# Kernel optimization log

Hardware: AMD Instinct MI355X
Metric: run time of the kernel (lower is better)

## Reference

```python
import jax, jax.numpy as jnp
import numpy as np

A, OBS, TD, H, M, ACT, AE = 1024, 2048, 256, 128, 16, 256, 64


def setup_inputs() -> dict:
    key = jax.random.key(0)
    ks = jax.random.split(key, 16)
    p = lambda k, shape: jax.random.normal(k, shape, dtype=jnp.float32) * 0.02
    obs = jax.random.normal(ks[0], (A, OBS), dtype=jnp.float32)
    # group membership matrix: exactly M members per initiator row (ATOC top-m groups)
    scores = jax.random.uniform(ks[1], (A, A))
    idx = jnp.argsort(scores, axis=1)[:, :M]
    C = jnp.zeros((A, A), dtype=bool).at[jnp.arange(A)[:, None], idx].set(True)
    inp = dict(obs=obs, C=C)
    # actor_1: Linear(OBS,TD) -> LN -> ReLU -> Linear(TD,TD) -> LN
    inp['W1'] = p(ks[2], (OBS, TD)); inp['b1'] = jnp.zeros((TD,), jnp.float32)
    inp['g1'] = jnp.ones((TD,), jnp.float32); inp['bt1'] = jnp.zeros((TD,), jnp.float32)
    inp['W2'] = p(ks[3], (TD, TD)); inp['b2'] = jnp.zeros((TD,), jnp.float32)
    inp['g2'] = jnp.ones((TD,), jnp.float32); inp['bt2'] = jnp.zeros((TD,), jnp.float32)
    # attention unit: 2-layer MLP + sigmoid head
    inp['aW1'] = p(ks[4], (TD, AE)); inp['ab1'] = jnp.zeros((AE,), jnp.float32)
    inp['aW2'] = p(ks[5], (AE, AE)); inp['ab2'] = jnp.zeros((AE,), jnp.float32)
    inp['aW3'] = p(ks[6], (AE, 1)); inp['ab3'] = jnp.zeros((1,), jnp.float32)
    # bi-directional LSTM (PyTorch layout: W_ih [4H,TD], W_hh [4H,H])
    inp['Wih_f'] = p(ks[7], (4 * H, TD)); inp['Whh_f'] = p(ks[8], (4 * H, H))
    inp['bih_f'] = jnp.zeros((4 * H,), jnp.float32); inp['bhh_f'] = jnp.zeros((4 * H,), jnp.float32)
    inp['Wih_r'] = p(ks[9], (4 * H, TD)); inp['Whh_r'] = p(ks[10], (4 * H, H))
    inp['bih_r'] = jnp.zeros((4 * H,), jnp.float32); inp['bhh_r'] = jnp.zeros((4 * H,), jnp.float32)
    # actor_2: ReLU -> Linear(TD,TD) -> LN -> Linear(TD,ACT) -> LN -> Tanh
    inp['W3'] = p(ks[11], (TD, TD)); inp['b3'] = jnp.zeros((TD,), jnp.float32)
    inp['g3'] = jnp.ones((TD,), jnp.float32); inp['bt3'] = jnp.zeros((TD,), jnp.float32)
    inp['W4'] = p(ks[12], (TD, ACT)); inp['b4'] = jnp.zeros((ACT,), jnp.float32)
    inp['g4'] = jnp.ones((ACT,), jnp.float32); inp['bt4'] = jnp.zeros((ACT,), jnp.float32)
    return inp


def _ln(x, g, b, eps=1e-5):
    m = jnp.mean(x, -1, keepdims=True)
    v = jnp.mean((x - m) ** 2, -1, keepdims=True)
    return (x - m) * jax.lax.rsqrt(v + eps) * g + b


def _lstm(seq, Wih, Whh, bih, bhh):
    # seq [T, D] -> hidden outputs [T, H]; PyTorch gate order i, f, g, o
    def step(carry, x):
        h, c = carry
        z = x @ Wih.T + bih + h @ Whh.T + bhh
        i, f, g, o = jnp.split(z, 4)
        c = jax.nn.sigmoid(f) * c + jax.nn.sigmoid(i) * jnp.tanh(g)
        h = jax.nn.sigmoid(o) * jnp.tanh(c)
        return (h, c), h
    h0 = jnp.zeros((H,), seq.dtype)
    _, hs = jax.lax.scan(step, (h0, h0), seq)
    return hs


def _forward(obs, C, W1, b1, g1, bt1, W2, b2, g2, bt2, aW1, ab1, aW2, ab2, aW3, ab3,
             Wih_f, Whh_f, bih_f, bhh_f, Wih_r, Whh_r, bih_r, bhh_r,
             W3, b3, g3, bt3, W4, b4, g4, bt4):
    # actor_1
    t = jax.nn.relu(_ln(obs @ W1 + b1, g1, bt1))
    thoughts = _ln(t @ W2 + b2, g2, bt2)  # [A, TD]
    # attention unit -> initiators (threshold 0.5)
    a = jax.nn.relu(thoughts @ aW1 + ab1)
    a = jax.nn.relu(a @ aW2 + ab2)
    init_prob = jax.nn.sigmoid(a @ aW3 + ab3)[:, 0]
    is_init = init_prob > 0.5  # [A]
    tpos = jnp.arange(M)

    def comm_step(th, xs):
        mask, active = xs
        # members first (stable, increasing agent index), padded gather of size M
        order = jnp.argsort((~mask).astype(jnp.int32))[:M]
        gcnt = jnp.sum(mask).astype(jnp.int32)
        seq_f = th[order]                        # [M, TD]
        rev = jnp.clip(gcnt - 1 - tpos, 0, M - 1)
        seq_b = seq_f[rev]                       # valid prefix reversed
        out_f = _lstm(seq_f, Wih_f, Whh_f, bih_f, bhh_f)
        out_b = _lstm(seq_b, Wih_r, Whh_r, bih_r, bhh_r)
        out = jnp.concatenate([out_f, out_b[rev]], axis=-1)  # [M, TD] bi-LSTM aligned
        valid = (tpos < gcnt) & active
        newv = jnp.where(valid[:, None], out, seq_f)         # merge = replace by integrated
        return th.at[order].set(newv), None

    thoughts, _ = jax.lax.scan(comm_step, thoughts, (C, is_init))
    # actor_2
    h = jax.nn.relu(thoughts)
    h = _ln(h @ W3 + b3, g3, bt3)
    acts = jnp.tanh(_ln(h @ W4 + b4, g4, bt4))
    return acts


def reference(obs, C, W1, b1, g1, bt1, W2, b2, g2, bt2, aW1, ab1, aW2, ab2, aW3, ab3,
              Wih_f, Whh_f, bih_f, bhh_f, Wih_r, Whh_r, bih_r, bhh_r,
              W3, b3, g3, bt3, W4, b4, g4, bt4):
    return _forward(obs, C, W1, b1, g1, bt1, W2, b2, g2, bt2, aW1, ab1, aW2, ab2, aW3, ab3,
                    Wih_f, Whh_f, bih_f, bhh_f, Wih_r, Whh_r, bih_r, bhh_r,
                    W3, b3, g3, bt3, W4, b4, g4, bt4)
```

## Files before the change

### kernel.cpp

```cpp
#include <hip/hip_runtime.h>
#include <cstdint>
#include <cstddef>
#include <math.h>

#define A_N   1024
#define OBS_N 2048
#define TD_N  256
#define H_N   128
#define M_N   16
#define AE_N  64
#define NWGC  32

typedef _Float16 h2 __attribute__((ext_vector_type(2)));
typedef _Float16 f16x8 __attribute__((ext_vector_type(8)));
typedef float f32x4 __attribute__((ext_vector_type(4)));

__device__ __forceinline__ float sigf(float x) { return 1.0f / (1.0f + expf(-x)); }
__device__ __forceinline__ h2 u2h(unsigned int u) { union { unsigned int x; h2 h; } c; c.x = u; return c.h; }
__device__ __forceinline__ unsigned int packh(float a, float b) {
  union { h2 h; unsigned int u; } c;
  c.h = (h2){(_Float16)a, (_Float16)b};
  return c.u;
}

__device__ __forceinline__ bool c_at(const unsigned char* C, int as_int, size_t idx) {
  return as_int ? (((const int*)C)[idx] != 0) : (C[idx] != 0);
}

__global__ __launch_bounds__(64) void k_cdet(const unsigned char* __restrict__ C, int* __restrict__ flag) {
  int lane = threadIdx.x;
  int cnt = 0;
  for (int i = lane; i < 4096; i += 64) cnt += (C[i] != 0) ? 1 : 0;
  for (int off = 32; off; off >>= 1) cnt += __shfl_down(cnt, off);
  if (lane == 0) flag[0] = (cnt < 40) ? 1 : 0;
}

__global__ __launch_bounds__(256) void k_actor1a(const float* __restrict__ obs,
    const float* __restrict__ W1, const float* __restrict__ b1,
    const float* __restrict__ g1, const float* __restrict__ bt1,
    float* __restrict__ tout) {
  __shared__ float S[4 * OBS_N];
  __shared__ float red[4][4][2];
  int tid = threadIdx.x;
  int r0 = blockIdx.x * 4;
  {
    const float4* src = (const float4*)(obs + (size_t)r0 * OBS_N);
    float4* dst = (float4*)S;
    for (int i = tid; i < 4 * OBS_N / 4; i += 256) dst[i] = src[i];
  }
  __syncthreads();
  int j = tid;
  float acc0 = 0, acc1 = 0, acc2 = 0, acc3 = 0;
  const float4* S4 = (const float4*)S;
  for (int k4 = 0; k4 < OBS_N / 4; k4++) {
    float w0 = W1[(k4 * 4 + 0) * TD_N + j];
    float w1 = W1[(k4 * 4 + 1) * TD_N + j];
    float w2 = W1[(k4 * 4 + 2) * TD_N + j];
    float w3 = W1[(k4 * 4 + 3) * TD_N + j];
    float4 s0 = S4[0 * 512 + k4], s1 = S4[1 * 512 + k4], s2 = S4[2 * 512 + k4], s3 = S4[3 * 512 + k4];
    acc0 += s0.x * w0 + s0.y * w1 + s0.z * w2 + s0.w * w3;
    acc1 += s1.x * w0 + s1.y * w1 + s1.z * w2 + s1.w * w3;
    acc2 += s2.x * w0 + s2.y * w1 + s2.z * w2 + s2.w * w3;
    acc3 += s3.x * w0 + s3.y * w1 + s3.z * w2 + s3.w * w3;
  }
  float z[4] = {acc0 + b1[j], acc1 + b1[j], acc2 + b1[j], acc3 + b1[j]};
  int w = tid >> 6, lane = tid & 63;
  for (int r = 0; r < 4; r++) {
    float v = z[r], v2 = z[r] * z[r];
    for (int off = 32; off; off >>= 1) { v += __shfl_down(v, off); v2 += __shfl_down(v2, off); }
    if (lane == 0) { red[r][w][0] = v; red[r][w][1] = v2; }
  }
  __syncthreads();
  for (int r = 0; r < 4; r++) {
    float sm = red[r][0][0] + red[r][1][0] + red[r][2][0] + red[r][3][0];
    float sq = red[r][0][1] + red[r][1][1] + red[r][2][1] + red[r][3][1];
    float mean = sm * (1.0f / TD_N);
    float var = sq * (1.0f / TD_N) - mean * mean;
    float rs = 1.0f / sqrtf(var + 1e-5f);
    float val = (z[r] - mean) * rs * g1[j] + bt1[j];
    tout[(size_t)(r0 + r) * TD_N + j] = fmaxf(val, 0.0f);
  }
}

__global__ __launch_bounds__(256) void k_actor1b(const float* __restrict__ tin,
    const float* __restrict__ W2, const float* __restrict__ b2,
    const float* __restrict__ g2, const float* __restrict__ bt2,
    float* __restrict__ th) {
  __shared__ float S[4 * TD_N];
  __shared__ float red[4][4][2];
  int tid = threadIdx.x;
  int r0 = blockIdx.x * 4;
  for (int i = tid; i < 4 * TD_N; i += 256) S[i] = tin[(size_t)r0 * TD_N + i];
  __syncthreads();
  int j = tid;
  float z[4] = {0, 0, 0, 0};
  const float4* S4 = (const float4*)S;
  for (int k4 = 0; k4 < TD_N / 4; k4++) {
    float w0 = W2[(k4 * 4 + 0) * TD_N + j];
    float w1 = W2[(k4 * 4 + 1) * TD_N + j];
    float w2v = W2[(k4 * 4 + 2) * TD_N + j];
    float w3 = W2[(k4 * 4 + 3) * TD_N + j];
#pragma unroll
    for (int r = 0; r < 4; r++) {
      float4 sv = S4[r * 64 + k4];
      z[r] += sv.x * w0 + sv.y * w1 + sv.z * w2v + sv.w * w3;
    }
  }
  for (int r = 0; r < 4; r++) z[r] += b2[j];
  int w = tid >> 6, lane = tid & 63;
  for (int r = 0; r < 4; r++) {
    float v = z[r], v2 = z[r] * z[r];
    for (int off = 32; off; off >>= 1) { v += __shfl_down(v, off); v2 += __shfl_down(v2, off); }
    if (lane == 0) { red[r][w][0] = v; red[r][w][1] = v2; }
  }
  __syncthreads();
  for (int r = 0; r < 4; r++) {
    float sm = red[r][0][0] + red[r][1][0] + red[r][2][0] + red[r][3][0];
    float sq = red[r][0][1] + red[r][1][1] + red[r][2][1] + red[r][3][1];
    float mean = sm * (1.0f / TD_N);
    float var = sq * (1.0f / TD_N) - mean * mean;
    float rs = 1.0f / sqrtf(var + 1e-5f);
    th[(size_t)(r0 + r) * TD_N + j] = (z[r] - mean) * rs * g2[j] + bt2[j];
  }
}

__global__ __launch_bounds__(256) void k_att(const float* __restrict__ th,
    const float* __restrict__ aW1, const float* __restrict__ ab1,
    const float* __restrict__ aW2, const float* __restrict__ ab2,
    const float* __restrict__ aW3, const float* __restrict__ ab3,
    int* __restrict__ isin) {
  __shared__ float S[4 * TD_N];
  __shared__ double A1[4 * AE_N];
  __shared__ double A2[4 * AE_N];
  int tid = threadIdx.x;
  int r0 = blockIdx.x * 4;
  for (int i = tid; i < 4 * TD_N; i += 256) S[i] = th[(size_t)r0 * TD_N + i];
  __syncthreads();
  int r = tid >> 6, c = tid & 63;
  double acc = 0;
  for (int k = 0; k < TD_N; k++) acc += (double)S[r * TD_N + k] * (double)aW1[k * AE_N + c];
  acc += (double)ab1[c];
  A1[r * AE_N + c] = acc > 0.0 ? acc : 0.0;
  __syncthreads();
  acc = 0;
  for (int k = 0; k < AE_N; k++) acc += A1[r * AE_N + k] * (double)aW2[k * AE_N + c];
  acc += (double)ab2[c];
  A2[r * AE_N + c] = acc > 0.0 ? acc : 0.0;
  __syncthreads();
  double p = A2[r * AE_N + c] * (double)aW3[c];
  for (int off = 32; off; off >>= 1) p += __shfl_down(p, off);
  if (c == 0) isin[r0 + r] = ((p + (double)ab3[0]) > 0.0) ? 1 : 0;
}

__global__ __launch_bounds__(64) void k_memb(const unsigned char* __restrict__ C,
    const int* __restrict__ flag, int* __restrict__ memb) {
  int s = blockIdx.x, lane = threadIdx.x;
  int as_int = flag[0];
  if (lane < M_N) memb[s * M_N + lane] = lane;
  __syncthreads();
  int base = 0;
  for (int ch = 0; ch < 16; ch++) {
    int col = ch * 64 + lane;
    bool v = c_at(C, as_int, (size_t)s * A_N + col);
    unsigned long long m = __ballot(v);
    if (v) {
      int pos = base + __popcll(m & ((1ull << lane) - 1ull));
      if (pos < M_N) memb[s * M_N + pos] = col;
    }
    base += __popcll(m);
  }
}

__global__ __launch_bounds__(256) void k_req(const unsigned char* __restrict__ C,
    const int* __restrict__ flag, const int* __restrict__ memb,
    const int* __restrict__ isin, int* __restrict__ req) {
  __shared__ int Ls[A_N];
  int s = blockIdx.x, tid = threadIdx.x;
  int as_int = flag[0];
  for (int i = tid; i < A_N; i += 256) Ls[i] = isin[i];
  __syncthreads();
  int i = tid >> 4, sub = tid & 15;
  int m = memb[s * M_N + i] & (A_N - 1);
  int cnt = 0;
  for (int s2 = sub; s2 < s; s2 += 16)
    if (Ls[s2] && c_at(C, as_int, (size_t)s2 * A_N + m)) cnt++;
  for (int off = 1; off < 16; off <<= 1) cnt += __shfl_xor(cnt, off);
  if (sub == 0) req[s * M_N + i] = cnt;
}

__global__ __launch_bounds__(256) void k_prep(
    const float* __restrict__ Wih_f, const float* __restrict__ Wih_r,
    const float* __restrict__ Whh_f, const float* __restrict__ Whh_r,
    const float* __restrict__ bih_f, const float* __restrict__ bhh_f,
    const float* __restrict__ bih_r, const float* __restrict__ bhh_r,
    unsigned int* __restrict__ wfragf, unsigned int* __restrict__ wfragr,
    unsigned int* __restrict__ whhpf, unsigned int* __restrict__ whhpr,
    float* __restrict__ bsumf, float* __restrict__ bsumr,
    int* __restrict__ verF, int* __restrict__ verB) {
  int id = blockIdx.x * 256 + threadIdx.x;
  if (id < 65536) {
    int j = id & 3, l = (id >> 2) & 63, tile = (id >> 8) & 31, c = id >> 13;
    int gate = tile * 16 + (l & 15);
    int k = c * 32 + ((l >> 4) << 3) + (j << 1);
    wfragf[id] = packh(Wih_f[gate * TD_N + k], Wih_f[gate * TD_N + k + 1]);
    wfragr[id] = packh(Wih_r[gate * TD_N + k], Wih_r[gate * TD_N + k + 1]);
  }
  if (id < 32768) {
    int g = id & 511, k2 = id >> 9;
    whhpf[id] = packh(Whh_f[g * H_N + 2 * k2], Whh_f[g * H_N + 2 * k2 + 1]);
    whhpr[id] = packh(Whh_r[g * H_N + 2 * k2], Whh_r[g * H_N + 2 * k2 + 1]);
  }
  if (id < 512) { bsumf[id] = bih_f[id] + bhh_f[id]; bsumr[id] = bih_r[id] + bhh_r[id]; }
  if (id < A_N) { verF[id] = 0; verB[id] = 0; }
}

__global__ __launch_bounds__(64) void k_lvl(const int* __restrict__ isin,
    const int* __restrict__ memb, int* __restrict__ fin,
    int* __restrict__ lstart, int* __restrict__ llist) {
  __shared__ int membS[A_N * M_N];
  __shared__ int last[A_N];
  __shared__ int cnt[A_N + 2];
  __shared__ int cur[A_N + 2];
  __shared__ short lvlS[A_N];
  __shared__ unsigned char isinS[A_N];
  __shared__ unsigned char cntm[A_N];
  int lane = threadIdx.x;
  for (int i = lane; i < A_N * M_N; i += 64) membS[i] = memb[i] & (A_N - 1);
  for (int i = lane; i < A_N; i += 64) {
    isinS[i] = (unsigned char)(isin[i] != 0);
    last[i] = 0; cntm[i] = 0; lvlS[i] = 0;
  }
  for (int l = lane; l < A_N + 2; l += 64) cnt[l] = 0;
  __syncthreads();
  for (int s = 0; s < A_N; s++) {
    if (isinS[s]) {
      int li = 0, m = 0;
      if (lane < 16) { m = membS[s * M_N + lane]; li = last[m]; }
#pragma unroll
      for (int off = 8; off; off >>= 1) li = max(li, __shfl_xor(li, off));
      int L = __shfl(li, 0) + 1;
      if (lane < 16) { last[m] = L; cntm[m]++; }
      if (lane == 0) { lvlS[s] = (short)L; cnt[L]++; }
    }
  }
  if (lane == 0) {
    int acc = 0;
    for (int L = 1; L <= A_N; L++) { cur[L] = acc; acc += cnt[L]; }
    lstart[0] = acc;
    for (int s = 0; s < A_N; s++) {
      int L = lvlS[s];
      if (L > 0) llist[cur[L]++] = s;
    }
  }
  for (int i = lane; i < A_N; i += 64) fin[i] = cntm[i] & 1;
}

#define RSH 264
__global__ __launch_bounds__(512)
void k_scan(
    float* __restrict__ thA, float* __restrict__ thB,
    const int* __restrict__ lstart, const int* __restrict__ llist,
    const int* __restrict__ memb, const int* __restrict__ req,
    int* __restrict__ verF, int* __restrict__ verB,
    const unsigned int* __restrict__ wfragf, const unsigned int* __restrict__ wfragr,
    const unsigned int* __restrict__ whhpf, const unsigned int* __restrict__ whhpr,
    const float* __restrict__ bsumf, const float* __restrict__ bsumr) {
  __shared__ __align__(16) unsigned short Sh[16 * RSH];
  __shared__ float xa_lds[16 * 512 + 7936];
  __shared__ float hh[16 * H_N];
  __shared__ float garr[4 * H_N];
  __shared__ unsigned int hp[2 * 64];
  __shared__ int memb_s[16];
  __shared__ int par_s[16];
  int tid = threadIdx.x;
  int wg = blockIdx.x;
  int dir = wg & 1;
  int pair = wg >> 1;
  int dmask = dir ? 15 : 0;
  const unsigned int* wfrag = dir ? wfragr : wfragf;
  const unsigned int* whhp = dir ? whhpr : whhpf;
  float blo = (dir ? bsumr : bsumf)[tid];
  int istanh = ((tid >> 7) == 2);
  int* vown = dir ? verB : verF;
  int wv = tid >> 6, lane = tid & 63;
  int fm = lane & 15, fkg = lane >> 4;
  unsigned int wreg[64];
#pragma unroll
  for (int k2 = 0; k2 < 64; k2++) wreg[k2] = whhp[k2 * 512 + tid];
#pragma unroll
  for (int k2 = 0; k2 < 64; k2++) asm volatile("" : "+v"(wreg[k2]));

  int nact = lstart[0];
  for (int idx = pair; idx < nact; idx += NWGC / 2) {
    int s = llist[idx];
    if (tid < 16) {
      int m = memb[s * M_N + tid] & (A_N - 1);
      int rq = req[s * M_N + tid];
      memb_s[tid] = m;
      par_s[tid] = rq & 1;
      int tries = 0;
      while (__hip_atomic_load(&verF[m], __ATOMIC_RELAXED, __HIP_MEMORY_SCOPE_AGENT) < rq ||
             __hip_atomic_load(&verB[m], __ATOMIC_RELAXED, __HIP_MEMORY_SCOPE_AGENT) < rq) {
        __builtin_amdgcn_s_sleep(2);
        if (++tries > (1 << 20)) break;
      }
    }
    __syncthreads();
    {
      int r = tid >> 5, p = tid & 31;
      int j = r ^ dmask;
      const float* src = (par_s[j] ? thB : thA) + (size_t)memb_s[j] * TD_N + p * 8;
      float v[8];
#pragma unroll
      for (int q = 0; q < 8; q++)
        v[q] = __hip_atomic_load(src + q, __ATOMIC_RELAXED, __HIP_MEMORY_SCOPE_AGENT);
      uint4 pk;
      pk.x = packh(v[0], v[1]); pk.y = packh(v[2], v[3]);
      pk.z = packh(v[4], v[5]); pk.w = packh(v[6], v[7]);
      *(uint4*)((char*)Sh + r * 528 + p * 16) = pk;
    }
    __syncthreads();
    {
#pragma unroll
      for (int t4 = 0; t4 < 4; t4++) {
        int tile = wv * 4 + t4;
        f32x4 acc = {0.0f, 0.0f, 0.0f, 0.0f};
#pragma unroll 2
        for (int c = 0; c < 8; c++) {
          f16x8 af = *(const f16x8*)((const char*)Sh + fm * 528 + c * 64 + fkg * 16);
          union { uint4 u; f16x8 h; } bu;
          bu.u = *(const uint4*)(wfrag + ((size_t)(c * 32 + tile) * 64 + lane) * 4);
          acc = __builtin_amdgcn_mfma_f32_16x16x32_f16(af, bu.h, acc, 0, 0, 0);
        }
#pragma unroll
        for (int r = 0; r < 4; r++)
          xa_lds[(fkg * 4 + r) * 512 + tile * 16 + fm] = acc[r];
      }
    }
    if (tid < 64) hp[tid] = 0u;
    float cst = 0.0f;
    __syncthreads();
#pragma unroll
    for (int u = 0; u < 16; u++) {
      float xau = xa_lds[u * 512 + tid] + blo;
      const uint4* hp4 = (const uint4*)(hp + (u & 1) * 64);
      float z0 = 0, z1 = 0, z2 = 0, z3 = 0;
#pragma unroll
      for (int j = 0; j < 16; j++) {
        uint4 hw = hp4[j];
        z0 = __builtin_amdgcn_fdot2(u2h(wreg[4 * j + 0]), u2h(hw.x), z0, false);
        z1 = __builtin_amdgcn_fdot2(u2h(wreg[4 * j + 1]), u2h(hw.y), z1, false);
        z2 = __builtin_amdgcn_fdot2(u2h(wreg[4 * j + 2]), u2h(hw.z), z2, false);
        z3 = __builtin_amdgcn_fdot2(u2h(wreg[4 * j + 3]), u2h(hw.w), z3, false);
      }
      float z = xau + (z0 + z1) + (z2 + z3);
      garr[tid] = istanh ? tanhf(z) : sigf(z);
      __syncthreads();
      if (tid < H_N) {
        cst = garr[H_N + tid] * cst + garr[tid] * garr[2 * H_N + tid];
        float hv = garr[3 * H_N + tid] * tanhf(cst);
        float hvn = __shfl_down(hv, 1);
        if (!(tid & 1)) hp[((u + 1) & 1) * 64 + (tid >> 1)] = packh(hv, hvn);
        hh[u * H_N + tid] = hv;
      }
      __syncthreads();
    }
#pragma unroll
    for (int q = 0; q < 4; q++) {
      int i2 = q * 512 + tid;
      int u = i2 >> 7, col = i2 & 127;
      int slot = u ^ dmask;
      float* dst = (par_s[slot] ? thA : thB) + (size_t)memb_s[slot] * TD_N + dir * H_N + col;
      __hip_atomic_store(dst, hh[u * H_N + col], __ATOMIC_RELAXED, __HIP_MEMORY_SCOPE_AGENT);
    }
    __syncthreads();
    if (tid < 16)
      __hip_atomic_fetch_add(&vown[memb_s[tid]], 1, __ATOMIC_RELAXED, __HIP_MEMORY_SCOPE_AGENT);
    __syncthreads();
  }
}

__global__ __launch_bounds__(256) void k_actor2(const float* __restrict__ thA, const float* __restrict__ thB,
    const int* __restrict__ fin,
    const float* __restrict__ W3, const float* __restrict__ b3,
    const float* __restrict__ g3, const float* __restrict__ bt3,
    const float* __restrict__ W4, const float* __restrict__ b4,
    const float* __restrict__ g4, const float* __restrict__ bt4,
    float* __restrict__ out) {
  __shared__ float Hs[4 * TD_N];
  __shared__ float H3[4 * TD_N];
  __shared__ float red[4][4][2];
  int tid = threadIdx.x;
  int r0 = blockIdx.x * 4;
  int j = tid;
  for (int i = tid; i < 4 * TD_N; i += 256) {
    int r = i >> 8, col = i & 255;
    int row = r0 + r;
    const float* src = (fin[row] ? thB : thA) + (size_t)row * TD_N + col;
    float v = __hip_atomic_load(src, __ATOMIC_RELAXED, __HIP_MEMORY_SCOPE_AGENT);
    Hs[i] = fmaxf(v, 0.0f);
  }
  __syncthreads();
  float z[4] = {0, 0, 0, 0};
  {
    const float4* S4 = (const float4*)Hs;
    for (int k4 = 0; k4 < 64; k4++) {
      float w0 = W3[(k4 * 4 + 0) * TD_N + j];
      float w1 = W3[(k4 * 4 + 1) * TD_N + j];
      float w2 = W3[(k4 * 4 + 2) * TD_N + j];
      float w3v = W3[(k4 * 4 + 3) * TD_N + j];
#pragma unroll
      for (int r = 0; r < 4; r++) {
        float4 sv = S4[r * 64 + k4];
        z[r] += sv.x * w0 + sv.y * w1 + sv.z * w2 + sv.w * w3v;
      }
    }
  }
  for (int r = 0; r < 4; r++) z[r] += b3[j];
  int w = tid >> 6, lane = tid & 63;
  for (int r = 0; r < 4; r++) {
    float v = z[r], v2 = z[r] * z[r];
    for (int off = 32; off; off >>= 1) { v += __shfl_down(v, off); v2 += __shfl_down(v2, off); }
    if (lane == 0) { red[r][w][0] = v; red[r][w][1] = v2; }
  }
  __syncthreads();
  for (int r = 0; r < 4; r++) {
    float sm = red[r][0][0] + red[r][1][0] + red[r][2][0] + red[r][3][0];
    float sq = red[r][0][1] + red[r][1][1] + red[r][2][1] + red[r][3][1];
    float mean = sm * (1.0f / TD_N);
    float var = sq * (1.0f / TD_N) - mean * mean;
    float rs = 1.0f / sqrtf(var + 1e-5f);
    H3[r * TD_N + j] = (z[r] - mean) * rs * g3[j] + bt3[j];
  }
  __syncthreads();
  float z2a[4] = {0, 0, 0, 0};
  {
    const float4* S4 = (const float4*)H3;
    for (int k4 = 0; k4 < 64; k4++) {
      float w0 = W4[(k4 * 4 + 0) * TD_N + j];
      float w1 = W4[(k4 * 4 + 1) * TD_N + j];
      float w2 = W4[(k4 * 4 + 2) * TD_N + j];
      float w3v = W4[(k4 * 4 + 3) * TD_N + j];
#pragma unroll
      for (int r = 0; r < 4; r++) {
        float4 sv = S4[r * 64 + k4];
        z2a[r] += sv.x * w0 + sv.y * w1 + sv.z * w2 + sv.w * w3v;
      }
    }
  }
  for (int r = 0; r < 4; r++) z2a[r] += b4[j];
  __syncthreads();
  for (int r = 0; r < 4; r++) {
    float v = z2a[r], v2 = z2a[r] * z2a[r];
    for (int off = 32; off; off >>= 1) { v += __shfl_down(v, off); v2 += __shfl_down(v2, off); }
    if (lane == 0) { red[r][w][0] = v; red[r][w][1] = v2; }
  }
  __syncthreads();
  for (int r = 0; r < 4; r++) {
    float sm = red[r][0][0] + red[r][1][0] + red[r][2][0] + red[r][3][0];
    float sq = red[r][0][1] + red[r][1][1] + red[r][2][1] + red[r][3][1];
    float mean = sm * (1.0f / TD_N);
    float var = sq * (1.0f / TD_N) - mean * mean;
    float rs = 1.0f / sqrtf(var + 1e-5f);
    float val = (z2a[r] - mean) * rs * g4[j] + bt4[j];
    out[(size_t)(r0 + r) * TD_N + j] = tanhf(val);
  }
}

extern "C" void kernel_launch(void* const* d_in, const int* in_sizes, int n_in,
                              void* d_out, int out_size, void* d_ws, size_t ws_size,
                              hipStream_t stream) {
  const float* obs = (const float*)d_in[0];
  const unsigned char* C = (const unsigned char*)d_in[1];
  const float* W1 = (const float*)d_in[2];  const float* b1 = (const float*)d_in[3];
  const float* g1 = (const float*)d_in[4];  const float* bt1 = (const float*)d_in[5];
  const float* W2 = (const float*)d_in[6];  const float* b2 = (const float*)d_in[7];
  const float* g2 = (const float*)d_in[8];  const float* bt2 = (const float*)d_in[9];
  const float* aW1 = (const float*)d_in[10]; const float* ab1 = (const float*)d_in[11];
  const float* aW2 = (const float*)d_in[12]; const float* ab2 = (const float*)d_in[13];
  const float* aW3 = (const float*)d_in[14]; const float* ab3 = (const float*)d_in[15];
  const float* Wih_f = (const float*)d_in[16]; const float* Whh_f = (const float*)d_in[17];
  const float* bih_f = (const float*)d_in[18]; const float* bhh_f = (const float*)d_in[19];
  const float* Wih_r = (const float*)d_in[20]; const float* Whh_r = (const float*)d_in[21];
  const float* bih_r = (const float*)d_in[22]; const float* bhh_r = (const float*)d_in[23];
  const float* W3 = (const float*)d_in[24]; const float* b3 = (const float*)d_in[25];
  const float* g3 = (const float*)d_in[26]; const float* bt3 = (const float*)d_in[27];
  const float* W4 = (const float*)d_in[28]; const float* b4 = (const float*)d_in[29];
  const float* g4 = (const float*)d_in[30]; const float* bt4 = (const float*)d_in[31];
  float* out = (float*)d_out;

  float* ws = (float*)d_ws;
  unsigned int* wfragf = (unsigned int*)ws;
  unsigned int* wfragr = (unsigned int*)(ws + 131072);
  unsigned int* whhpf = (unsigned int*)(ws + 262144);
  unsigned int* whhpr = (unsigned int*)(ws + 327680);
  float* bsumf = ws + 393216;
  float* bsumr = ws + 393728;
  float* thB   = ws + 394240;
  float* t_buf = ws + 394240;
  int* ibase   = (int*)(ws + 656384);
  int* membi   = ibase;
  int* reqi    = ibase + 16384;
  int* isin    = ibase + 32768;
  int* flag    = ibase + 33792;
  int* fin     = ibase + 33856;
  int* lstart  = ibase + 34880;
  int* llist   = ibase + 34944;
  int* verF    = ibase + 35968;
  int* verB    = ibase + 36992;
  size_t need = (size_t)(656384 + 38016 + 64) * 4;
  if (ws_size < need) return;

  (void)in_sizes; (void)n_in; (void)out_size;

  float* thA = out;

  k_cdet<<<1, 64, 0, stream>>>(C, flag);
  k_actor1a<<<256, 256, 0, stream>>>(obs, W1, b1, g1, bt1, t_buf);
  k_actor1b<<<256, 256, 0, stream>>>(t_buf, W2, b2, g2, bt2, thA);
  k_att<<<256, 256, 0, stream>>>(thA, aW1, ab1, aW2, ab2, aW3, ab3, isin);
  k_memb<<<1024, 64, 0, stream>>>(C, flag, membi);
  k_req<<<1024, 256, 0, stream>>>(C, flag, membi, isin, reqi);
  k_prep<<<512, 256, 0, stream>>>(Wih_f, Wih_r, Whh_f, Whh_r, bih_f, bhh_f, bih_r, bhh_r,
                                  wfragf, wfragr, whhpf, whhpr, bsumf, bsumr, verF, verB);
  k_lvl<<<1, 64, 0, stream>>>(isin, membi, fin, lstart, llist);
  k_scan<<<NWGC, 512, 0, stream>>>(thA, thB, lstart, llist, membi, reqi, verF, verB,
                                   wfragf, wfragr, whhpf, whhpr, bsumf, bsumr);
  k_actor2<<<256, 256, 0, stream>>>(thA, thB, fin, W3, b3, g3, bt3, W4, b4, g4, bt4, out);
}
```

Before: 4.896 ms.

## Publish LSTM outputs and version counters per timestep instead of after the sequence

The bi-LSTM scan kernel now writes each timestep's hidden state straight to global memory and bumps that member's version counter right after the step. Before, it staged all 16 steps in LDS and published them together at the end. Groups waiting on a member can therefore start earlier, cutting the critical path of the cross-workgroup dependency chain. The recurrent dot product is also split across eight independent accumulators for more instruction-level parallelism, and the spin-wait sleep is shortened. In exchange, global stores and atomics are issued once per step inside the recurrent loop, and visibility still relies on relaxed atomics with no explicit fence.

Measured after the change: 4.648 ms. -5.1%, faster.

```diff
diff --git a/kernel.cpp b/kernel.cpp
--- a/kernel.cpp
+++ b/kernel.cpp
@@ -266,8 +266,7 @@
     const unsigned int* __restrict__ whhpf, const unsigned int* __restrict__ whhpr,
     const float* __restrict__ bsumf, const float* __restrict__ bsumr) {
   __shared__ __align__(16) unsigned short Sh[16 * RSH];
-  __shared__ float xa_lds[16 * 512 + 7936];
-  __shared__ float hh[16 * H_N];
+  __shared__ float xa_lds[16 * 512 + 9984];
   __shared__ float garr[4 * H_N];
   __shared__ unsigned int hp[2 * 64];
   __shared__ int memb_s[16];
@@ -301,8 +300,8 @@
       int tries = 0;
       while (__hip_atomic_load(&verF[m], __ATOMIC_RELAXED, __HIP_MEMORY_SCOPE_AGENT) < rq ||
              __hip_atomic_load(&verB[m], __ATOMIC_RELAXED, __HIP_MEMORY_SCOPE_AGENT) < rq) {
-        __builtin_amdgcn_s_sleep(2);
-        if (++tries > (1 << 20)) break;
+        __builtin_amdgcn_s_sleep(1);
+        if (++tries > (1 << 21)) break;
       }
     }
     __syncthreads();
@@ -344,39 +343,36 @@
     for (int u = 0; u < 16; u++) {
       float xau = xa_lds[u * 512 + tid] + blo;
       const uint4* hp4 = (const uint4*)(hp + (u & 1) * 64);
-      float z0 = 0, z1 = 0, z2 = 0, z3 = 0;
-#pragma unroll
-      for (int j = 0; j < 16; j++) {
-        uint4 hw = hp4[j];
-        z0 = __builtin_amdgcn_fdot2(u2h(wreg[4 * j + 0]), u2h(hw.x), z0, false);
-        z1 = __builtin_amdgcn_fdot2(u2h(wreg[4 * j + 1]), u2h(hw.y), z1, false);
-        z2 = __builtin_amdgcn_fdot2(u2h(wreg[4 * j + 2]), u2h(hw.z), z2, false);
-        z3 = __builtin_amdgcn_fdot2(u2h(wreg[4 * j + 3]), u2h(hw.w), z3, false);
+      float z0 = 0, z1 = 0, z2 = 0, z3 = 0, z4 = 0, z5 = 0, z6 = 0, z7 = 0;
+#pragma unroll
+      for (int j = 0; j < 16; j += 2) {
+        uint4 ha = hp4[j], hb = hp4[j + 1];
+        z0 = __builtin_amdgcn_fdot2(u2h(wreg[4 * j + 0]), u2h(ha.x), z0, false);
+        z1 = __builtin_amdgcn_fdot2(u2h(wreg[4 * j + 1]), u2h(ha.y), z1, false);
+        z2 = __builtin_amdgcn_fdot2(u2h(wreg[4 * j + 2]), u2h(ha.z), z2, false);
+        z3 = __builtin_amdgcn_fdot2(u2h(wreg[4 * j + 3]), u2h(ha.w), z3, false);
+        z4 = __builtin_amdgcn_fdot2(u2h(wreg[4 * j + 4]), u2h(hb.x), z4, false);
+        z5 = __builtin_amdgcn_fdot2(u2h(wreg[4 * j + 5]), u2h(hb.y), z5, false);
+        z6 = __builtin_amdgcn_fdot2(u2h(wreg[4 * j + 6]), u2h(hb.z), z6, false);
+        z7 = __builtin_amdgcn_fdot2(u2h(wreg[4 * j + 7]), u2h(hb.w), z7, false);
       }
-      float z = xau + (z0 + z1) + (z2 + z3);
+      float z = xau + ((z0 + z1) + (z2 + z3)) + ((z4 + z5) + (z6 + z7));
       garr[tid] = istanh ? tanhf(z) : sigf(z);
       __syncthreads();
+      int r2 = u ^ dmask;
       if (tid < H_N) {
         cst = garr[H_N + tid] * cst + garr[tid] * garr[2 * H_N + tid];
         float hv = garr[3 * H_N + tid] * tanhf(cst);
         float hvn = __shfl_down(hv, 1);
         if (!(tid & 1)) hp[((u + 1) & 1) * 64 + (tid >> 1)] = packh(hv, hvn);
-        hh[u * H_N + tid] = hv;
+        float* dst = par_s[r2] ? thA : thB;
+        __hip_atomic_store(dst + (size_t)memb_s[r2] * TD_N + dir * H_N + tid, hv,
+                           __ATOMIC_RELAXED, __HIP_MEMORY_SCOPE_AGENT);
       }
       __syncthreads();
-    }
-#pragma unroll
-    for (int q = 0; q < 4; q++) {
-      int i2 = q * 512 + tid;
-      int u = i2 >> 7, col = i2 & 127;
-      int slot = u ^ dmask;
-      float* dst = (par_s[slot] ? thA : thB) + (size_t)memb_s[slot] * TD_N + dir * H_N + col;
-      __hip_atomic_store(dst, hh[u * H_N + col], __ATOMIC_RELAXED, __HIP_MEMORY_SCOPE_AGENT);
-    }
-    __syncthreads();
-    if (tid < 16)
-      __hip_atomic_fetch_add(&vown[memb_s[tid]], 1, __ATOMIC_RELAXED, __HIP_MEMORY_SCOPE_AGENT);
-    __syncthreads();
+      if (tid == 0)
+        __hip_atomic_fetch_add(&vown[memb_s[r2]], 1, __ATOMIC_RELAXED, __HIP_MEMORY_SCOPE_AGENT);
+    }
   }
 }
 
```
